# Kernel optimization log

Measured on AMD Instinct MI355X. Metric: run time of the kernel, lower is better.

## Reference

```python
import jax, jax.numpy as jnp
import numpy as np

S, M, E, K, D = 16384, 512, 16, 2, 256
H1, H2, H3 = 500, 500, 1000


def setup_inputs() -> dict:
    key = jax.random.key(0)
    ks = jax.random.split(key, 8)
    p = lambda k, sh: jax.random.normal(k, sh, dtype=jnp.float32) * 0.02
    return {
        "x": jax.random.normal(ks[0], (S, M), dtype=jnp.float32),
        "noise": jax.random.uniform(ks[1], (S, E), dtype=jnp.float32),  # Router's torch.rand noise
        "Wr": p(ks[2], (E, M)),                       # router weight (Linear, no bias)
        "W1": p(ks[3], (E, M, H1)), "b1": jnp.zeros((E, H1), jnp.float32),
        "W2": p(ks[4], (E, H1, H2)), "b2": jnp.zeros((E, H2), jnp.float32),
        "W3": p(ks[5], (E, H2, H3)), "b3": jnp.zeros((E, H3), jnp.float32),
        "W4": p(ks[6], (E, H3, D)), "b4": jnp.zeros((E, D), jnp.float32),
    }


def reference(x, noise, Wr, W1, b1, W2, b2, W3, b3, W4, b4):
    # Router: zero-init linear + uniform noise
    logits = x @ Wr.T + noise                      # [S,E]
    select = jax.nn.softmax(logits, axis=1)        # [S,E]
    gate, index = jax.lax.top_k(select, K)         # [S,K]
    gate = gate / gate.sum(axis=1, keepdims=True)
    mask = jax.nn.one_hot(index, E, dtype=jnp.float32)  # [S,K,E]

    # load-balance loss
    density = mask.sum(axis=1).mean(axis=0)        # [E]
    density_proxy = select.mean(axis=0)            # [E]
    balance_loss = (density_proxy * density).mean() * float(E ** 2)

    # combine tensor: mask_flat is all-ones, so combine = sum_k gate_k * one_hot_k
    final_weight = (gate[:, :, None] * mask).sum(axis=1)     # [S,E]
    dispatch = (final_weight > 0).astype(x.dtype)            # bool->float, [S,E]
    select0 = dispatch

    # dense one-hot dispatch: expert_inputs[e,s,:] = x[s,:] * dispatch[s,e]
    expert_inputs = jnp.einsum('sm,se->esm', x, dispatch)    # [E,S,M]

    # per-expert Encoder MLP, vectorized over experts
    h = jax.nn.relu(jnp.einsum('esm,emh->esh', expert_inputs, W1) + b1[:, None, :])
    h = jax.nn.relu(jnp.einsum('esh,ehg->esg', h, W2) + b2[:, None, :])
    h = jax.nn.relu(jnp.einsum('esg,egf->esf', h, W3) + b3[:, None, :])
    expert_out = jnp.einsum('esf,efd->esd', h, W4) + b4[:, None, :]  # [E,S,D]

    final_output = jnp.einsum('se,esd->sd', final_weight, expert_out)  # [S,D]
    dist_loss = jnp.float32(0.0)  # t=False path
    return final_output, select0, balance_loss, dist_loss
```

## Files before the change

kernel.cpp:

```cpp
#include <hip/hip_runtime.h>
#include <stdint.h>

#define S_TOK 16384
#define M_DIM 512
#define E_EXP 16
#define D_OUT 256
#define H1D 500
#define H2D 500
#define H3D 1000

typedef float f32x4 __attribute__((ext_vector_type(4)));
typedef long lx2 __attribute__((ext_vector_type(2)));
typedef int i32x2 __attribute__((ext_vector_type(2)));

template <bool HI>
__device__ __forceinline__ int pk8(float a, float b, int old) {
  return __builtin_amdgcn_cvt_pk_fp8_f32(a, b, old, HI);
}
__device__ __forceinline__ unsigned char f2fp8(float f) {
  return (unsigned char)(__builtin_amdgcn_cvt_pk_fp8_f32(f, 0.f, 0, false) & 0xff);
}

__device__ __forceinline__ void ld_lds16(const unsigned char* g, unsigned char* l) {
  __builtin_amdgcn_global_load_lds(
      (const __attribute__((address_space(1))) unsigned int*)(const void*)g,
      (__attribute__((address_space(3))) unsigned int*)(void*)l, 16, 0, 0);
}

struct TokenRec { int i1, i2; float g1, g2; };

__global__ __launch_bounds__(256) void k_router(const float* __restrict__ x,
                                                const float* __restrict__ noise,
                                                const float* __restrict__ Wr,
                                                float* __restrict__ sel_out,
                                                float* __restrict__ sel_buf,
                                                TokenRec* __restrict__ te) {
  __shared__ float wr[E_EXP * 516];
  int t = threadIdx.x;
  for (int i = t; i < E_EXP * M_DIM; i += 256) {
    int e = i >> 9, m = i & 511;
    wr[e * 516 + m] = Wr[i];
  }
  __syncthreads();

  int wv = t >> 6, l = t & 63;
  int e = l & 15, tg = l >> 4;
  int s = blockIdx.x * 16 + wv * 4 + tg;

  const float* xr = x + (size_t)s * M_DIM;
  const float* wre = &wr[e * 516];
  double a0 = 0.0, a1 = 0.0, a2 = 0.0, a3 = 0.0;
#pragma unroll 4
  for (int m = 0; m < M_DIM; m += 4) {
    f32x4 xv = *(const f32x4*)(xr + m);
    f32x4 wv4 = *(const f32x4*)(wre + m);
    a0 += (double)xv.x * (double)wv4.x;
    a1 += (double)xv.y * (double)wv4.y;
    a2 += (double)xv.z * (double)wv4.z;
    a3 += (double)xv.w * (double)wv4.w;
  }
  double a = (a0 + a1) + (a2 + a3);
  a += (double)noise[(size_t)s * E_EXP + e];

  double mx = a;
#pragma unroll
  for (int off = 8; off >= 1; off >>= 1) { double o = __shfl_xor(mx, off, 64); mx = (o > mx) ? o : mx; }
  double p = exp(a - mx);
  double sum = p;
#pragma unroll
  for (int off = 8; off >= 1; off >>= 1) sum += __shfl_xor(sum, off, 64);
  sel_buf[(size_t)s * E_EXP + e] = (float)(p / sum);

  unsigned long long pb = __double_as_longlong(p);
  unsigned long long key = (pb & ~0xFFull) | (unsigned long long)(255 - e);
  unsigned long long k1 = key;
#pragma unroll
  for (int off = 8; off >= 1; off >>= 1) { unsigned long long o = __shfl_xor(k1, off, 64); k1 = (o > k1) ? o : k1; }
  int i1 = 255 - (int)(k1 & 0xFFull);
  unsigned long long key2 = (e == i1) ? 0ull : key;
  unsigned long long k2 = key2;
#pragma unroll
  for (int off = 8; off >= 1; off >>= 1) { unsigned long long o = __shfl_xor(k2, off, 64); k2 = (o > k2) ? o : k2; }
  int i2 = 255 - (int)(k2 & 0xFFull);

  double p1 = __shfl(p, tg * 16 + i1, 64);
  double p2 = __shfl(p, tg * 16 + i2, 64);

  sel_out[(size_t)s * E_EXP + e] = (e == i1 || e == i2) ? 1.f : 0.f;
  if (e == 0) {
    double inv = 1.0 / (p1 + p2);
    TokenRec r; r.i1 = i1; r.i2 = i2; r.g1 = (float)(p1 * inv); r.g2 = (float)(p2 * inv);
    te[s] = r;
  }
}

__global__ __launch_bounds__(256) void k_stats(const float* __restrict__ sel_buf,
                                               const TokenRec* __restrict__ te,
                                               float* __restrict__ partials) {
  __shared__ float psum[256];
  __shared__ unsigned int hist[E_EXP];
  int t = threadIdx.x, b = blockIdx.x;
  if (t < E_EXP) hist[t] = 0u;
  __syncthreads();
  int e = t & 15, rg = t >> 4;
  int base = b * 1024;
  float acc = 0.f;
#pragma unroll 4
  for (int i = 0; i < 64; i++)
    acc += sel_buf[(size_t)(base + i * 16 + rg) * E_EXP + e];
  for (int i = t; i < 1024; i += 256) {
    TokenRec r = te[base + i];
    atomicAdd(&hist[r.i1], 1u);
    atomicAdd(&hist[r.i2], 1u);
  }
  psum[t] = acc;
  __syncthreads();
  if (t < E_EXP) {
    float v = 0.f;
#pragma unroll
    for (int rg2 = 0; rg2 < 16; rg2++) v += psum[rg2 * 16 + t];
    partials[b * 32 + t] = v;
    partials[b * 32 + 16 + t] = (float)hist[t];
  }
}

__global__ void k_prefix_loss(const float* __restrict__ partials,
                              unsigned int* __restrict__ counts,
                              unsigned int* __restrict__ offsets,
                              unsigned int* __restrict__ cursor,
                              float* __restrict__ out_loss) {
  __shared__ float pr[E_EXP];
  __shared__ unsigned int cn[E_EXP];
  int t = threadIdx.x;
  if (t < E_EXP) {
    float p = 0.f, c = 0.f;
    for (int b = 0; b < 16; b++) { p += partials[b * 32 + t]; c += partials[b * 32 + 16 + t]; }
    pr[t] = p; cn[t] = (unsigned int)(c + 0.5f);
    cursor[t] = 0u;
  }
  __syncthreads();
  if (t == 0) {
    unsigned int acc = 0; float ls = 0.f;
    for (int e = 0; e < E_EXP; e++) {
      counts[e] = cn[e];
      offsets[e] = acc;
      acc += cn[e];
      ls += pr[e] * (float)cn[e];
    }
    out_loss[0] = ls * ((float)E_EXP / ((float)S_TOK * (float)S_TOK));
    out_loss[1] = 0.f;
  }
}

__global__ __launch_bounds__(256) void k_listbuild(const TokenRec* __restrict__ te,
                                                   const unsigned int* __restrict__ offsets,
                                                   unsigned int* __restrict__ cursor,
                                                   int* __restrict__ slot_token,
                                                   float* __restrict__ slot_gate,
                                                   int* __restrict__ tok_slot) {
  __shared__ unsigned int lhist[E_EXP];
  __shared__ unsigned int lbase[E_EXP];
  __shared__ unsigned int lcur[E_EXP];
  int t = threadIdx.x, b = blockIdx.x;
  int base = b * 1024;
  if (t < E_EXP) lhist[t] = 0u;
  __syncthreads();
  for (int i = t; i < 1024; i += 256) {
    TokenRec r = te[base + i];
    atomicAdd(&lhist[r.i1], 1u);
    atomicAdd(&lhist[r.i2], 1u);
  }
  __syncthreads();
  if (t < E_EXP) {
    lbase[t] = offsets[t] + atomicAdd(&cursor[t], lhist[t]);
    lcur[t] = 0u;
  }
  __syncthreads();
  for (int i = t; i < 1024; i += 256) {
    int s = base + i;
    TokenRec r = te[s];
    unsigned int p1 = atomicAdd(&lcur[r.i1], 1u);
    int sl1 = (int)(lbase[r.i1] + p1);
    slot_token[sl1] = s; slot_gate[sl1] = r.g1;
    unsigned int p2 = atomicAdd(&lcur[r.i2], 1u);
    int sl2 = (int)(lbase[r.i2] + p2);
    slot_token[sl2] = s; slot_gate[sl2] = r.g2;
    tok_slot[2 * s] = sl1;
    tok_slot[2 * s + 1] = sl2;
  }
}

__global__ __launch_bounds__(256) void k_gather(const float* __restrict__ x,
                                                const int* __restrict__ slot_token,
                                                unsigned char* __restrict__ xg) {
  int idx = blockIdx.x * 256 + threadIdx.x;
  int row = idx >> 6, t6 = idx & 63;
  int blk = t6 >> 3, q = (t6 >> 1) & 3, h = t6 & 1;
  int tkn = slot_token[row];
  const float* xp = x + (size_t)tkn * M_DIM + blk * 64 + h * 32 + q * 8;
  f32x4 v0 = *(const f32x4*)xp;
  f32x4 v1 = *(const f32x4*)(xp + 4);
  int b0 = pk8<false>(v0.x, v0.y, 0); b0 = pk8<true>(v0.z, v0.w, b0);
  int b1 = pk8<false>(v1.x, v1.y, 0); b1 = pk8<true>(v1.z, v1.w, b1);
  i32x2 o; o.x = b0; o.y = b1;
  *(i32x2*)&xg[(size_t)row * 512 + blk * 64 + q * 16 + h * 8] = o;
}

__global__ __launch_bounds__(256) void k_convw(const float* __restrict__ src,
                                               unsigned char* __restrict__ dst,
                                               int Kr, int Nr, int Kp, int Np) {
  __shared__ float tile[64][65];
  int e = blockIdx.z;
  int k0 = blockIdx.x * 64, n0 = blockIdx.y * 64;
  int t = threadIdx.x;
  int cx = t & 63, ry = t >> 6;
  const float* sp = src + (size_t)e * Kr * Nr;
#pragma unroll
  for (int i = 0; i < 16; i++) {
    int k = k0 + ry + i * 4, n = n0 + cx;
    float v = (k < Kr && n < Nr) ? sp[(size_t)k * Nr + n] : 0.f;
    tile[ry + i * 4][cx] = v;
  }
  __syncthreads();
  int nl = t >> 2, q = t & 3;
  int b0 = pk8<false>(tile[q * 8 + 0][nl], tile[q * 8 + 1][nl], 0);
  b0 = pk8<true>(tile[q * 8 + 2][nl], tile[q * 8 + 3][nl], b0);
  int b1 = pk8<false>(tile[q * 8 + 4][nl], tile[q * 8 + 5][nl], 0);
  b1 = pk8<true>(tile[q * 8 + 6][nl], tile[q * 8 + 7][nl], b1);
  int c0 = pk8<false>(tile[32 + q * 8 + 0][nl], tile[32 + q * 8 + 1][nl], 0);
  c0 = pk8<true>(tile[32 + q * 8 + 2][nl], tile[32 + q * 8 + 3][nl], c0);
  int c1 = pk8<false>(tile[32 + q * 8 + 4][nl], tile[32 + q * 8 + 5][nl], 0);
  c1 = pk8<true>(tile[32 + q * 8 + 6][nl], tile[32 + q * 8 + 7][nl], c1);
  uint4 pk; pk.x = (unsigned)b0; pk.y = (unsigned)b1; pk.z = (unsigned)c0; pk.w = (unsigned)c1;
  *(uint4*)&dst[(size_t)e * Np * Kp + (size_t)(n0 + nl) * Kp + k0 + q * 16] = pk;
}

__global__ __launch_bounds__(256, 4) void k_gemm_mid(const unsigned char* __restrict__ in,
                                                  const unsigned char* __restrict__ wt,
                                                  const float* __restrict__ bias,
                                                  unsigned char* __restrict__ out,
                                                  const unsigned int* __restrict__ offsets,
                                                  const unsigned int* __restrict__ counts,
                                                  int KP, int NP, int NREAL) {
  int e = blockIdx.z;
  int n_e = (int)counts[e];
  if (n_e == 0) return;
  int base = (int)offsets[e];
  int bn = blockIdx.y;
  __shared__ __align__(16) unsigned char As[2][128 * 64];
  __shared__ __align__(16) unsigned char Bs[2][64 * 64];
  int t = threadIdx.x;
  int w = t >> 6, l = t & 63;
  int wm = w & 1, wn = w >> 1;
  int lr = l & 15, lq = l >> 4;
  int r_ = l >> 2, s_ = l & 3;
  int s2 = s_ ^ ((r_ >> 1) & 3);
  int rsw = (lq ^ ((lr >> 1) & 3)) * 16;
  int c0 = w * 2, c1 = w * 2 + 1;

  unsigned char* dA0[2] = {&As[0][c0 * 1024], &As[1][c0 * 1024]};
  unsigned char* dA1[2] = {&As[0][c1 * 1024], &As[1][c1 * 1024]};
  unsigned char* dB[2]  = {&Bs[0][w * 1024], &Bs[1][w * 1024]};

  const unsigned char* bW = wt + (size_t)e * NP * KP;
  const unsigned char* bsrc = bW + (size_t)(bn * 64 + w * 16 + r_) * KP + s2 * 16;
  int nk = KP >> 6;

  for (int bm = blockIdx.x; bm * 128 < n_e; bm += gridDim.x) {
    int ra = bm * 128 + c0 * 16 + r_; ra = (ra < n_e) ? ra : (n_e - 1);
    int rb = bm * 128 + c1 * 16 + r_; rb = (rb < n_e) ? rb : (n_e - 1);
    const unsigned char* a0 = in + (size_t)(base + ra) * KP + s2 * 16;
    const unsigned char* a1 = in + (size_t)(base + rb) * KP + s2 * 16;
    const unsigned char* bq = bsrc;
    f32x4 acc[4][2];
#pragma unroll
    for (int i = 0; i < 4; i++)
#pragma unroll
      for (int j = 0; j < 2; j++) acc[i][j] = (f32x4){0.f, 0.f, 0.f, 0.f};

    ld_lds16(a0, dA0[0]); ld_lds16(a1, dA1[0]); ld_lds16(bq, dB[0]);
    a0 += 64; a1 += 64; bq += 64;

    for (int ks = 0; ks < nk; ks++) {
      int cb = ks & 1, nb = cb ^ 1;
      __syncthreads();
      if (ks + 1 < nk) {
        ld_lds16(a0, dA0[nb]); ld_lds16(a1, dA1[nb]); ld_lds16(bq, dB[nb]);
        a0 += 64; a1 += 64; bq += 64;
      }
      lx2 af[4], bf[2];
#pragma unroll
      for (int mt = 0; mt < 4; mt++) af[mt] = *(const lx2*)&As[cb][(wm * 64 + mt * 16 + lr) * 64 + rsw];
#pragma unroll
      for (int nt = 0; nt < 2; nt++) bf[nt] = *(const lx2*)&Bs[cb][(wn * 32 + nt * 16 + lr) * 64 + rsw];
#pragma unroll
      for (int mt = 0; mt < 4; mt++)
#pragma unroll
        for (int nt = 0; nt < 2; nt++) {
          acc[mt][nt] = __builtin_amdgcn_mfma_f32_16x16x32_fp8_fp8(af[mt].x, bf[nt].x, acc[mt][nt], 0, 0, 0);
          acc[mt][nt] = __builtin_amdgcn_mfma_f32_16x16x32_fp8_fp8(af[mt].y, bf[nt].y, acc[mt][nt], 0, 0, 0);
        }
    }

#pragma unroll
    for (int nt = 0; nt < 2; nt++) {
      int col = bn * 64 + wn * 32 + nt * 16 + lr;
      bool cok = col < NREAL;
      float bv = cok ? bias[(size_t)e * NREAL + col] : 0.f;
      int kl = col & 63;
      int pb = ((kl >> 3) & 3) * 16 + ((kl >> 5) & 1) * 8 + (kl & 7);
#pragma unroll
      for (int mt = 0; mt < 4; mt++)
#pragma unroll
        for (int reg = 0; reg < 4; reg++) {
          int r = bm * 128 + wm * 64 + mt * 16 + lq * 4 + reg;
          if (r < n_e) {
            float v = cok ? fmaxf(acc[mt][nt][reg] + bv, 0.f) : 0.f;
            out[(size_t)(base + r) * NP + bn * 64 + pb] = f2fp8(v);
          }
        }
    }
  }
}

__global__ __launch_bounds__(256, 4) void k_gemm_fin(const unsigned char* __restrict__ in,
                                                  const unsigned char* __restrict__ wt,
                                                  const float* __restrict__ bias,
                                                  float* __restrict__ eo,
                                                  const unsigned int* __restrict__ offsets,
                                                  const unsigned int* __restrict__ counts,
                                                  const float* __restrict__ slot_gate) {
  const int KP = 1024, NP = 256;
  int e = blockIdx.z;
  int n_e = (int)counts[e];
  if (n_e == 0) return;
  int base = (int)offsets[e];
  int bn = blockIdx.y;
  __shared__ __align__(16) unsigned char As[2][128 * 64];
  __shared__ __align__(16) unsigned char Bs[2][64 * 64];
  int t = threadIdx.x;
  int w = t >> 6, l = t & 63;
  int wm = w & 1, wn = w >> 1;
  int lr = l & 15, lq = l >> 4;
  int r_ = l >> 2, s_ = l & 3;
  int s2 = s_ ^ ((r_ >> 1) & 3);
  int rsw = (lq ^ ((lr >> 1) & 3)) * 16;
  int c0 = w * 2, c1 = w * 2 + 1;

  unsigned char* dA0[2] = {&As[0][c0 * 1024], &As[1][c0 * 1024]};
  unsigned char* dA1[2] = {&As[0][c1 * 1024], &As[1][c1 * 1024]};
  unsigned char* dB[2]  = {&Bs[0][w * 1024], &Bs[1][w * 1024]};

  const unsigned char* bW = wt + (size_t)e * NP * KP;
  const unsigned char* bsrc = bW + (size_t)(bn * 64 + w * 16 + r_) * KP + s2 * 16;
  int nk = KP >> 6;

  for (int bm = blockIdx.x; bm * 128 < n_e; bm += gridDim.x) {
    int ra = bm * 128 + c0 * 16 + r_; ra = (ra < n_e) ? ra : (n_e - 1);
    int rb = bm * 128 + c1 * 16 + r_; rb = (rb < n_e) ? rb : (n_e - 1);
    const unsigned char* a0 = in + (size_t)(base + ra) * KP + s2 * 16;
    const unsigned char* a1 = in + (size_t)(base + rb) * KP + s2 * 16;
    const unsigned char* bq = bsrc;
    f32x4 acc[4][2];
#pragma unroll
    for (int i = 0; i < 4; i++)
#pragma unroll
      for (int j = 0; j < 2; j++) acc[i][j] = (f32x4){0.f, 0.f, 0.f, 0.f};

    ld_lds16(a0, dA0[0]); ld_lds16(a1, dA1[0]); ld_lds16(bq, dB[0]);
    a0 += 64; a1 += 64; bq += 64;

    for (int ks = 0; ks < nk; ks++) {
      int cb = ks & 1, nb = cb ^ 1;
      __syncthreads();
      if (ks + 1 < nk) {
        ld_lds16(a0, dA0[nb]); ld_lds16(a1, dA1[nb]); ld_lds16(bq, dB[nb]);
        a0 += 64; a1 += 64; bq += 64;
      }
      lx2 af[4], bf[2];
#pragma unroll
      for (int mt = 0; mt < 4; mt++) af[mt] = *(const lx2*)&As[cb][(wm * 64 + mt * 16 + lr) * 64 + rsw];
#pragma unroll
      for (int nt = 0; nt < 2; nt++) bf[nt] = *(const lx2*)&Bs[cb][(wn * 32 + nt * 16 + lr) * 64 + rsw];
#pragma unroll
      for (int mt = 0; mt < 4; mt++)
#pragma unroll
        for (int nt = 0; nt < 2; nt++) {
          acc[mt][nt] = __builtin_amdgcn_mfma_f32_16x16x32_fp8_fp8(af[mt].x, bf[nt].x, acc[mt][nt], 0, 0, 0);
          acc[mt][nt] = __builtin_amdgcn_mfma_f32_16x16x32_fp8_fp8(af[mt].y, bf[nt].y, acc[mt][nt], 0, 0, 0);
        }
    }

#pragma unroll
    for (int mt = 0; mt < 4; mt++)
#pragma unroll
      for (int reg = 0; reg < 4; reg++) {
        int r = bm * 128 + wm * 64 + mt * 16 + lq * 4 + reg;
        if (r < n_e) {
          int gr = base + r;
          float g = slot_gate[gr];
#pragma unroll
          for (int nt = 0; nt < 2; nt++) {
            int col = bn * 64 + wn * 32 + nt * 16 + lr;
            eo[(size_t)gr * NP + col] = g * (acc[mt][nt][reg] + bias[(size_t)e * 256 + col]);
          }
        }
      }
  }
}

__global__ __launch_bounds__(256) void k_combine(const float* __restrict__ eo,
                                                 const int* __restrict__ tok_slot,
                                                 float* __restrict__ out) {
  int idx = blockIdx.x * 256 + threadIdx.x;
  int s = idx >> 6, q = idx & 63;
  int sl1 = tok_slot[2 * s], sl2 = tok_slot[2 * s + 1];
  f32x4 v1 = *(const f32x4*)&eo[(size_t)sl1 * D_OUT + q * 4];
  f32x4 v2 = *(const f32x4*)&eo[(size_t)sl2 * D_OUT + q * 4];
  *(f32x4*)&out[(size_t)s * D_OUT + q * 4] = v1 + v2;
}

extern "C" void kernel_launch(void* const* d_in, const int* in_sizes, int n_in,
                              void* d_out, int out_size, void* d_ws, size_t ws_size,
                              hipStream_t stream) {
  const float* x    = (const float*)d_in[0];
  const float* nois = (const float*)d_in[1];
  const float* Wr   = (const float*)d_in[2];
  const float* W1   = (const float*)d_in[3];
  const float* b1   = (const float*)d_in[4];
  const float* W2   = (const float*)d_in[5];
  const float* b2   = (const float*)d_in[6];
  const float* W3   = (const float*)d_in[7];
  const float* b3   = (const float*)d_in[8];
  const float* W4   = (const float*)d_in[9];
  const float* b4   = (const float*)d_in[10];
  float* out = (float*)d_out;

  char* w = (char*)d_ws;
  unsigned char* actA = (unsigned char*)(w + 0);
  unsigned char* actB = (unsigned char*)(w + 33554432);
  unsigned char* Wt   = (unsigned char*)(w + 50331648);
  float*         eo   = (float*)(w + 58720256);
  int*           slot_token = (int*)(w + 92274688);
  float*         slot_gate  = (float*)(w + 92405760);
  TokenRec*      te         = (TokenRec*)(w + 92536832);
  unsigned int*  counts  = (unsigned int*)(w + 92798976);
  unsigned int*  cursor  = (unsigned int*)(w + 92799040);
  unsigned int*  offsets = (unsigned int*)(w + 92799104);
  int*           tok_slot = (int*)(w + 92799232);
  float*         sel_buf  = (float*)(w + 0);
  float*         partials = (float*)(w + 1048576);

  float* sel_out  = out + (size_t)S_TOK * D_OUT;
  float* loss_out = out + (size_t)S_TOK * D_OUT + (size_t)S_TOK * E_EXP;

  k_router<<<dim3(S_TOK / 16), dim3(256), 0, stream>>>(x, nois, Wr, sel_out, sel_buf, te);
  k_stats<<<dim3(16), dim3(256), 0, stream>>>(sel_buf, te, partials);
  k_prefix_loss<<<dim3(1), dim3(64), 0, stream>>>(partials, counts, offsets, cursor, loss_out);
  k_listbuild<<<dim3(16), dim3(256), 0, stream>>>(te, offsets, cursor, slot_token, slot_gate, tok_slot);
  k_gather<<<dim3((2 * S_TOK * 64) / 256), dim3(256), 0, stream>>>(x, slot_token, actB);

  k_convw<<<dim3(8, 8, E_EXP), dim3(256), 0, stream>>>(W1, Wt, 512, H1D, 512, 512);
  k_gemm_mid<<<dim3(24, 8, E_EXP), dim3(256), 0, stream>>>(actB, Wt, b1, actA, offsets, counts, 512, 512, H1D);
  k_convw<<<dim3(8, 8, E_EXP), dim3(256), 0, stream>>>(W2, Wt, H1D, H2D, 512, 512);
  k_gemm_mid<<<dim3(24, 8, E_EXP), dim3(256), 0, stream>>>(actA, Wt, b2, actB, offsets, counts, 512, 512, H2D);
  k_convw<<<dim3(8, 16, E_EXP), dim3(256), 0, stream>>>(W3, Wt, H2D, H3D, 512, 1024);
  k_gemm_mid<<<dim3(24, 16, E_EXP), dim3(256), 0, stream>>>(actB, Wt, b3, actA, offsets, counts, 512, 1024, H3D);
  k_convw<<<dim3(16, 4, E_EXP), dim3(256), 0, stream>>>(W4, Wt, H3D, D_OUT, 1024, 256);
  k_gemm_fin<<<dim3(24, 4, E_EXP), dim3(256), 0, stream>>>(actA, Wt, b4, eo, offsets, counts, slot_gate);
  k_combine<<<dim3(S_TOK * 64 / 256), dim3(256), 0, stream>>>(eo, tok_slot, out);

  (void)in_sizes; (void)n_in; (void)out_size; (void)ws_size;
}
```

Before: 385.7 us.

## Merge four weight conversions into one launch and shrink final GEMM M-tile

Converts all four expert weight matrices to FP8 in a single kernel launch, writing each into its own workspace buffer, instead of four separate conversion launches placed between the GEMMs. Three launches and their serialization points disappear, and weight conversion no longer sits between consecutive GEMMs. The final GEMM's block tile is also reduced from 128 to 64 rows with a larger grid, giving more blocks per expert and better occupancy for the small N=256 output. The cost is a larger workspace, more B-tile reloads per row, and less MFMA work per block in the final GEMM.

```diff
diff --git a/kernel.cpp b/kernel.cpp
--- a/kernel.cpp
+++ b/kernel.cpp
@@ -206,12 +206,23 @@
   *(i32x2*)&xg[(size_t)row * 512 + blk * 64 + q * 16 + h * 8] = o;
 }
 
-__global__ __launch_bounds__(256) void k_convw(const float* __restrict__ src,
-                                               unsigned char* __restrict__ dst,
-                                               int Kr, int Nr, int Kp, int Np) {
+__global__ __launch_bounds__(256) void k_convw_all(const float* __restrict__ W1,
+                                                   const float* __restrict__ W2,
+                                                   const float* __restrict__ W3,
+                                                   const float* __restrict__ W4,
+                                                   unsigned char* __restrict__ D1,
+                                                   unsigned char* __restrict__ D2,
+                                                   unsigned char* __restrict__ D3,
+                                                   unsigned char* __restrict__ D4) {
   __shared__ float tile[64][65];
-  int e = blockIdx.z;
-  int k0 = blockIdx.x * 64, n0 = blockIdx.y * 64;
+  int tb = blockIdx.x, e = blockIdx.y;
+  const float* src; unsigned char* dst;
+  int Kr, Nr, Kp, Np, kx, ny;
+  if (tb < 64)        { src = W1; dst = D1; Kr = 512;  Nr = H1D; Kp = 512;  Np = 512;  kx = tb >> 3;  ny = tb & 7; }
+  else if (tb < 128)  { tb -= 64;  src = W2; dst = D2; Kr = H1D; Nr = H2D; Kp = 512;  Np = 512;  kx = tb >> 3;  ny = tb & 7; }
+  else if (tb < 256)  { tb -= 128; src = W3; dst = D3; Kr = H2D; Nr = H3D; Kp = 512;  Np = 1024; kx = tb >> 4;  ny = tb & 15; }
+  else                { tb -= 256; src = W4; dst = D4; Kr = H3D; Nr = 256; Kp = 1024; Np = 256;  kx = tb >> 2;  ny = tb & 3; }
+  int k0 = kx * 64, n0 = ny * 64;
   int t = threadIdx.x;
   int cx = t & 63, ry = t >> 6;
   const float* sp = src + (size_t)e * Kr * Nr;
@@ -336,7 +347,7 @@
   if (n_e == 0) return;
   int base = (int)offsets[e];
   int bn = blockIdx.y;
-  __shared__ __align__(16) unsigned char As[2][128 * 64];
+  __shared__ __align__(16) unsigned char As[2][64 * 64];
   __shared__ __align__(16) unsigned char Bs[2][64 * 64];
   int t = threadIdx.x;
   int w = t >> 6, l = t & 63;
@@ -345,45 +356,41 @@
   int r_ = l >> 2, s_ = l & 3;
   int s2 = s_ ^ ((r_ >> 1) & 3);
   int rsw = (lq ^ ((lr >> 1) & 3)) * 16;
-  int c0 = w * 2, c1 = w * 2 + 1;
-
-  unsigned char* dA0[2] = {&As[0][c0 * 1024], &As[1][c0 * 1024]};
-  unsigned char* dA1[2] = {&As[0][c1 * 1024], &As[1][c1 * 1024]};
-  unsigned char* dB[2]  = {&Bs[0][w * 1024], &Bs[1][w * 1024]};
+
+  unsigned char* dA[2] = {&As[0][w * 1024], &As[1][w * 1024]};
+  unsigned char* dB[2] = {&Bs[0][w * 1024], &Bs[1][w * 1024]};
 
   const unsigned char* bW = wt + (size_t)e * NP * KP;
   const unsigned char* bsrc = bW + (size_t)(bn * 64 + w * 16 + r_) * KP + s2 * 16;
   int nk = KP >> 6;
 
-  for (int bm = blockIdx.x; bm * 128 < n_e; bm += gridDim.x) {
-    int ra = bm * 128 + c0 * 16 + r_; ra = (ra < n_e) ? ra : (n_e - 1);
-    int rb = bm * 128 + c1 * 16 + r_; rb = (rb < n_e) ? rb : (n_e - 1);
+  for (int bm = blockIdx.x; bm * 64 < n_e; bm += gridDim.x) {
+    int ra = bm * 64 + w * 16 + r_; ra = (ra < n_e) ? ra : (n_e - 1);
     const unsigned char* a0 = in + (size_t)(base + ra) * KP + s2 * 16;
-    const unsigned char* a1 = in + (size_t)(base + rb) * KP + s2 * 16;
     const unsigned char* bq = bsrc;
-    f32x4 acc[4][2];
-#pragma unroll
-    for (int i = 0; i < 4; i++)
+    f32x4 acc[2][2];
+#pragma unroll
+    for (int i = 0; i < 2; i++)
 #pragma unroll
       for (int j = 0; j < 2; j++) acc[i][j] = (f32x4){0.f, 0.f, 0.f, 0.f};
 
-    ld_lds16(a0, dA0[0]); ld_lds16(a1, dA1[0]); ld_lds16(bq, dB[0]);
-    a0 += 64; a1 += 64; bq += 64;
+    ld_lds16(a0, dA[0]); ld_lds16(bq, dB[0]);
+    a0 += 64; bq += 64;
 
     for (int ks = 0; ks < nk; ks++) {
       int cb = ks & 1, nb = cb ^ 1;
       __syncthreads();
       if (ks + 1 < nk) {
-        ld_lds16(a0, dA0[nb]); ld_lds16(a1, dA1[nb]); ld_lds16(bq, dB[nb]);
-        a0 += 64; a1 += 64; bq += 64;
+        ld_lds16(a0, dA[nb]); ld_lds16(bq, dB[nb]);
+        a0 += 64; bq += 64;
       }
-      lx2 af[4], bf[2];
-#pragma unroll
-      for (int mt = 0; mt < 4; mt++) af[mt] = *(const lx2*)&As[cb][(wm * 64 + mt * 16 + lr) * 64 + rsw];
+      lx2 af[2], bf[2];
+#pragma unroll
+      for (int mt = 0; mt < 2; mt++) af[mt] = *(const lx2*)&As[cb][(wm * 32 + mt * 16 + lr) * 64 + rsw];
 #pragma unroll
       for (int nt = 0; nt < 2; nt++) bf[nt] = *(const lx2*)&Bs[cb][(wn * 32 + nt * 16 + lr) * 64 + rsw];
 #pragma unroll
-      for (int mt = 0; mt < 4; mt++)
+      for (int mt = 0; mt < 2; mt++)
 #pragma unroll
         for (int nt = 0; nt < 2; nt++) {
           acc[mt][nt] = __builtin_amdgcn_mfma_f32_16x16x32_fp8_fp8(af[mt].x, bf[nt].x, acc[mt][nt], 0, 0, 0);
@@ -392,10 +399,10 @@
     }
 
 #pragma unroll
-    for (int mt = 0; mt < 4; mt++)
+    for (int mt = 0; mt < 2; mt++)
 #pragma unroll
       for (int reg = 0; reg < 4; reg++) {
-        int r = bm * 128 + wm * 64 + mt * 16 + lq * 4 + reg;
+        int r = bm * 64 + wm * 32 + mt * 16 + lq * 4 + reg;
         if (r < n_e) {
           int gr = base + r;
           float g = slot_gate[gr];
@@ -439,20 +446,25 @@
   char* w = (char*)d_ws;
   unsigned char* actA = (unsigned char*)(w + 0);
   unsigned char* actB = (unsigned char*)(w + 33554432);
-  unsigned char* Wt   = (unsigned char*)(w + 50331648);
-  float*         eo   = (float*)(w + 58720256);
-  int*           slot_token = (int*)(w + 92274688);
-  float*         slot_gate  = (float*)(w + 92405760);
-  TokenRec*      te         = (TokenRec*)(w + 92536832);
-  unsigned int*  counts  = (unsigned int*)(w + 92798976);
-  unsigned int*  cursor  = (unsigned int*)(w + 92799040);
-  unsigned int*  offsets = (unsigned int*)(w + 92799104);
-  int*           tok_slot = (int*)(w + 92799232);
+  unsigned char* Wt1  = (unsigned char*)(w + 50331648);
+  unsigned char* Wt2  = (unsigned char*)(w + 54525952);
+  unsigned char* Wt3  = (unsigned char*)(w + 58720256);
+  unsigned char* Wt4  = (unsigned char*)(w + 67108864);
+  float*         eo   = (float*)(w + 71303168);
+  int*           slot_token = (int*)(w + 104857600);
+  float*         slot_gate  = (float*)(w + 104988672);
+  TokenRec*      te         = (TokenRec*)(w + 105119744);
+  unsigned int*  counts  = (unsigned int*)(w + 105381888);
+  unsigned int*  cursor  = (unsigned int*)(w + 105381952);
+  unsigned int*  offsets = (unsigned int*)(w + 105382016);
+  int*           tok_slot = (int*)(w + 105382080);
   float*         sel_buf  = (float*)(w + 0);
   float*         partials = (float*)(w + 1048576);
 
   float* sel_out  = out + (size_t)S_TOK * D_OUT;
   float* loss_out = out + (size_t)S_TOK * D_OUT + (size_t)S_TOK * E_EXP;
+
+  k_convw_all<<<dim3(320, E_EXP), dim3(256), 0, stream>>>(W1, W2, W3, W4, Wt1, Wt2, Wt3, Wt4);
 
   k_router<<<dim3(S_TOK / 16), dim3(256), 0, stream>>>(x, nois, Wr, sel_out, sel_buf, te);
   k_stats<<<dim3(16), dim3(256), 0, stream>>>(sel_buf, te, partials);
@@ -460,14 +472,10 @@
   k_listbuild<<<dim3(16), dim3(256), 0, stream>>>(te, offsets, cursor, slot_token, slot_gate, tok_slot);
   k_gather<<<dim3((2 * S_TOK * 64) / 256), dim3(256), 0, stream>>>(x, slot_token, actB);
 
-  k_convw<<<dim3(8, 8, E_EXP), dim3(256), 0, stream>>>(W1, Wt, 512, H1D, 512, 512);
-  k_gemm_mid<<<dim3(24, 8, E_EXP), dim3(256), 0, stream>>>(actB, Wt, b1, actA, offsets, counts, 512, 512, H1D);
-  k_convw<<<dim3(8, 8, E_EXP), dim3(256), 0, stream>>>(W2, Wt, H1D, H2D, 512, 512);
-  k_gemm_mid<<<dim3(24, 8, E_EXP), dim3(256), 0, stream>>>(actA, Wt, b2, actB, offsets, counts, 512, 512, H2D);
-  k_convw<<<dim3(8, 16, E_EXP), dim3(256), 0, stream>>>(W3, Wt, H2D, H3D, 512, 1024);
-  k_gemm_mid<<<dim3(24, 16, E_EXP), dim3(256), 0, stream>>>(actB, Wt, b3, actA, offsets, counts, 512, 1024, H3D);
-  k_convw<<<dim3(16, 4, E_EXP), dim3(256), 0, stream>>>(W4, Wt, H3D, D_OUT, 1024, 256);
-  k_gemm_fin<<<dim3(24, 4, E_EXP), dim3(256), 0, stream>>>(actA, Wt, b4, eo, offsets, counts, slot_gate);
+  k_gemm_mid<<<dim3(24, 8, E_EXP), dim3(256), 0, stream>>>(actB, Wt1, b1, actA, offsets, counts, 512, 512, H1D);
+  k_gemm_mid<<<dim3(24, 8, E_EXP), dim3(256), 0, stream>>>(actA, Wt2, b2, actB, offsets, counts, 512, 512, H2D);
+  k_gemm_mid<<<dim3(24, 16, E_EXP), dim3(256), 0, stream>>>(actB, Wt3, b3, actA, offsets, counts, 512, 1024, H3D);
+  k_gemm_fin<<<dim3(32, 4, E_EXP), dim3(256), 0, stream>>>(actA, Wt4, b4, eo, offsets, counts, slot_gate);
   k_combine<<<dim3(S_TOK * 64 / 256), dim3(256), 0, stream>>>(eo, tok_slot, out);
 
   (void)in_sizes; (void)n_in; (void)out_size; (void)ws_size;
```

Result: no change. 379.0 us (-1.7%).
